# Performance work log

Measured on AMD Instinct MI355X. Metric: run time of the kernel, lower is better.

## Reference

```python
import jax, jax.numpy as jnp
import numpy as np

RADII = (0.8, 1.6)
NSAMPLES = (16, 32)
NUM_GRIDPOINTS = 216


def rotate_z(points, theta):
    # points (b, n, m, 3), theta (b, n); rotate xy about z-axis
    c = jnp.cos(theta)[:, :, None]
    s = jnp.sin(theta)[:, :, None]
    x, y, z = points[..., 0], points[..., 1], points[..., 2]
    return jnp.stack([c * x - s * y, s * x + c * y, z], axis=-1)


def ball_query(d2, radius, nsample):
    # d2: (b, Ng, K) squared distances. Returns first nsample in-radius point
    # indices per query (CUDA ball_query semantics: pad with first found index,
    # 0 if none found).
    K = d2.shape[-1]
    ar = jnp.arange(K, dtype=jnp.int32)
    scores = jnp.where(d2 < radius * radius, ar, K)  # K == sentinel for 'not in ball'
    idx = -jax.lax.top_k(-scores, nsample)[0]        # nsample smallest => first hits, ascending
    first = idx[..., :1]
    idx = jnp.where(idx >= K, first, idx)
    idx = jnp.where(idx >= K, 0, idx)
    return idx


def gather_group(xyz, feats_t, new_xyz, idx):
    # xyz (b,K,3), feats_t (b,K,C), new_xyz (b,Ng,3), idx (b,Ng,ns)
    gx = jax.vmap(lambda p, i: p[i])(xyz, idx)      # (b,Ng,ns,3)
    gf = jax.vmap(lambda f, i: f[i])(feats_t, idx)  # (b,Ng,ns,C)
    rel = gx - new_xyz[:, :, None, :]               # use_xyz=True relative coords
    return jnp.concatenate([rel, gf], axis=-1)      # (b,Ng,ns,3+C)


def setup_inputs() -> dict:
    key = jax.random.key(0)
    ks = jax.random.split(key, 12)
    b, n, m, K, C = 2, 48, NUM_GRIDPOINTS, 2048, 128
    proposals = jax.random.uniform(ks[0], (b, n, 7), dtype=jnp.float32)
    keypoint_xyz = jax.random.normal(ks[1], (b, K, 3), dtype=jnp.float32)
    keypoint_features = jax.random.normal(ks[2], (b, C, K), dtype=jnp.float32)
    grid_noise = jax.random.uniform(ks[3], (b, n, m, 3), dtype=jnp.float32)

    def lin(k, o, i):
        return jax.random.normal(k, (o, i), dtype=jnp.float32) / np.float32(np.sqrt(i))

    w0_0 = lin(ks[4], 64, C + 3)
    w0_1 = lin(ks[5], 64, 64)
    w1_0 = lin(ks[6], 64, C + 3)
    w1_1 = lin(ks[7], 64, 64)
    red_w0 = lin(ks[8], 256, 128 * m)
    red_w1 = lin(ks[9], 256, 256)
    z64 = jnp.zeros((64,), jnp.float32)
    return {
        'proposals': proposals, 'keypoint_xyz': keypoint_xyz,
        'keypoint_features': keypoint_features, 'grid_noise': grid_noise,
        'w0_0': w0_0, 'b0_0': z64, 'w0_1': w0_1, 'b0_1': z64,
        'w1_0': w1_0, 'b1_0': z64, 'w1_1': w1_1, 'b1_1': z64,
        'red_w0': red_w0, 'red_b0': jnp.zeros((256,), jnp.float32),
        'red_w1': red_w1, 'red_b1': jnp.zeros((256,), jnp.float32),
    }


def reference(proposals, keypoint_xyz, keypoint_features, grid_noise,
              w0_0, b0_0, w0_1, b0_1, w1_0, b1_0, w1_1, b1_1,
              red_w0, red_b0, red_w1, red_b1):
    b, n, _ = proposals.shape
    m = NUM_GRIDPOINTS
    # sample_gridpoints: uniform in box dims, rotate by yaw, shift to center
    grid = grid_noise * proposals[:, :, None, 3:6]
    grid = rotate_z(grid, proposals[..., 6]) + proposals[:, :, None, 0:3]
    new_xyz = grid.reshape(b, n * m, 3)                      # (b, Ng, 3)
    # squared pairwise distances via |a|^2 + |b|^2 - 2ab (avoids (b,Ng,K,3) temp)
    d2 = (jnp.sum(new_xyz * new_xyz, -1)[:, :, None]
          + jnp.sum(keypoint_xyz * keypoint_xyz, -1)[:, None, :]
          - 2.0 * jnp.einsum('bnd,bkd->bnk', new_xyz, keypoint_xyz))
    feats_t = jnp.transpose(keypoint_features, (0, 2, 1))    # (b, K, C)
    scale_params = [((w0_0, b0_0), (w0_1, b0_1)), ((w1_0, b1_0), (w1_1, b1_1))]
    outs = []
    for radius, ns, layers in zip(RADII, NSAMPLES, scale_params):
        idx = ball_query(d2, radius, ns)                     # (b, Ng, ns)
        x = gather_group(keypoint_xyz, feats_t, new_xyz, idx)  # (b, Ng, ns, 3+C)
        for W, bias in layers:                               # shared 1x1-conv MLP (BN folded)
            x = jax.nn.relu(jnp.einsum('bnsc,oc->bnso', x, W) + bias)
        outs.append(jnp.max(x, axis=2))                      # max-pool over neighbors
    x = jnp.concatenate(outs, axis=-1)                       # (b, Ng, Cout)
    Cout = x.shape[-1]
    # (b, Cout, n, m).permute(0,2,1,3).view(b, n, Cout*m) equivalent
    x = x.reshape(b, n, m, Cout).transpose(0, 1, 3, 2).reshape(b, n, Cout * m)
    x = jax.nn.relu(x @ red_w0.T + red_b0)
    x = jax.nn.relu(x @ red_w1.T + red_b1)
    return x
```

## Files before the change

kernel.cpp:

```cpp
#include <hip/hip_runtime.h>
#include <cstdint>

#define NPROP  48
#define MGRID  216
#define NPT    (NPROP*MGRID)
#define KPT    2048
#define CFEAT  128
#define R0SQ   0.64f
#define R1SQ   2.56f
#define NS0    16
#define NS1    32
#define KRED   (CFEAT*MGRID)
#define NPOINTS (2*NPT)

typedef float f32x4  __attribute__((ext_vector_type(4)));
typedef short bf16x8 __attribute__((ext_vector_type(8)));

#define AFRAG_OFF 0
#define HID_SZ    (96*256)
#define HID_OFF   8192
#define Q0_OFF    (HID_OFF + HID_SZ)
#define POOL_OFF  (Q0_OFF + 4*KPT*64)
#define W0T_OFF   (POOL_OFF + NPOINTS*CFEAT)

__device__ __forceinline__ unsigned short bf_rne(float x) {
    unsigned u = __float_as_uint(x);
    return (unsigned short)((u + 0x7fffu + ((u >> 16) & 1u)) >> 16);
}
__device__ __forceinline__ float bf_f32(unsigned short h) {
    return __uint_as_float(((unsigned)h) << 16);
}

__global__ __launch_bounds__(64) void k_wfrag(
    const float* __restrict__ w01, const float* __restrict__ w11,
    float* __restrict__ ws)
{
    int bid = blockIdx.x;
    int kc = bid & 1, ot = (bid >> 1) & 3, s = bid >> 3;
    const float* W = s ? w11 : w01;
    int l   = threadIdx.x;
    int row = ot*16 + (l & 15);
    int k0  = kc*32 + (l >> 4)*8;
    union { unsigned short u16[8]; bf16x8 v; } hh, hl;
#pragma unroll
    for (int j = 0; j < 8; ++j) {
        float x  = W[row*64 + k0 + j];
        unsigned short hi = bf_rne(x);
        float xl = x - bf_f32(hi);
        hh.u16[j] = hi;
        hl.u16[j] = bf_rne(xl);
    }
    bf16x8* Ahi = (bf16x8*)(ws + AFRAG_OFF);
    bf16x8* Alo = Ahi + 16*64;
    int fi = (s*4 + ot)*2 + kc;
    Ahi[fi*64 + l] = hh.v;
    Alo[fi*64 + l] = hl.v;
}

template <int W>
__device__ __forceinline__ void wtr_tile(const float* __restrict__ src,
                                         float* __restrict__ dst,
                                         float* __restrict__ t, int g0)
{
    const int stride = W + 1;
    for (int idx = threadIdx.x; idx < 128*W; idx += 256) {
        int c = idx / W, gg = idx - c*W;
        t[c*stride + gg] = src[c*216 + g0 + gg];
    }
    __syncthreads();
    for (int idx = threadIdx.x; idx < 128*W; idx += 256) {
        int gg = idx >> 7, c = idx & 127;
        dst[(size_t)(g0+gg)*128 + c] = t[c*stride + gg];
    }
    __syncthreads();
}

__global__ __launch_bounds__(256) void k_wtr(
    const float* __restrict__ rw0, float* __restrict__ ws)
{
    __shared__ float t[128*65];
    int o = blockIdx.x;
    const float* src = rw0 + (size_t)o*KRED;
    float* dst = ws + W0T_OFF + (size_t)o*KRED;
    wtr_tile<64>(src, dst, t, 0);
    wtr_tile<64>(src, dst, t, 64);
    wtr_tile<64>(src, dst, t, 128);
    wtr_tile<24>(src, dst, t, 192);
}

__global__ __launch_bounds__(256) void k_qproj(
    const float* __restrict__ kxyz, const float* __restrict__ feats,
    const float* __restrict__ w0, const float* __restrict__ b0,
    const float* __restrict__ w1, const float* __restrict__ b1,
    float* __restrict__ ws)
{
    __shared__ float wl[64*131];
    int bid  = blockIdx.x;
    int kgrp = bid & 511;
    int s    = (bid >> 9) & 1;
    int b    = bid >> 10;
    const float* W    = s ? w1 : w0;
    const float* bias = s ? b1 : b0;
    for (int i = threadIdx.x; i < 64*131; i += 256) wl[i] = W[i];
    __syncthreads();
    int k = kgrp*4 + (threadIdx.x >> 6);
    int o = threadIdx.x & 63;
    float acc = bias[o];
    const float* kp = kxyz + ((size_t)b*KPT + k)*3;
    acc = fmaf(wl[o*131+0], kp[0], acc);
    acc = fmaf(wl[o*131+1], kp[1], acc);
    acc = fmaf(wl[o*131+2], kp[2], acc);
    const float* f = feats + (size_t)b*CFEAT*KPT + k;
#pragma unroll 8
    for (int c = 0; c < CFEAT; ++c)
        acc = fmaf(wl[o*131+3+c], f[(size_t)c*KPT], acc);
    ws[Q0_OFF + (size_t)s*(2*KPT*64) + ((size_t)b*KPT + k)*64 + o] = acc;
}

template <int NST>
__device__ __forceinline__ void mfma_tail(
    const float* __restrict__ Qb, const bf16x8* __restrict__ Ahi,
    const bf16x8* __restrict__ Alo, const float* __restrict__ bs,
    const int* __restrict__ idxl, const float* __restrict__ u_lds,
    float* __restrict__ stage, int sbase, int lane)
{
    const int g = lane >> 4;
    bf16x8 Bhi[NST][2], Blo[NST][2];
#pragma unroll
    for (int st = 0; st < NST; ++st) {
        int sp = idxl[st*16 + (lane & 15)];
        const float* qr = Qb + ((size_t)sp << 6) + g*8;
#pragma unroll
        for (int kc = 0; kc < 2; ++kc) {
            f32x4 q0 = *(const f32x4*)(qr + kc*32);
            f32x4 q1 = *(const f32x4*)(qr + kc*32 + 4);
            f32x4 u0 = *(const f32x4*)(u_lds + kc*32 + g*8);
            f32x4 u1 = *(const f32x4*)(u_lds + kc*32 + g*8 + 4);
            union { unsigned short u16[8]; bf16x8 v; } hh, hl;
#pragma unroll
            for (int j = 0; j < 4; ++j) {
                float x = fmaxf(q0[j] - u0[j], 0.f);
                unsigned short hi = bf_rne(x);
                hh.u16[j] = hi;
                hl.u16[j] = bf_rne(x - bf_f32(hi));
                float y = fmaxf(q1[j] - u1[j], 0.f);
                unsigned short hi2 = bf_rne(y);
                hh.u16[j+4] = hi2;
                hl.u16[j+4] = bf_rne(y - bf_f32(hi2));
            }
            Bhi[st][kc] = hh.v;
            Blo[st][kc] = hl.v;
        }
    }
#pragma unroll
    for (int ot = 0; ot < 4; ++ot) {
        int fi = (sbase + ot)*2;
        bf16x8 ah0 = Ahi[(fi+0)*64 + lane];
        bf16x8 ah1 = Ahi[(fi+1)*64 + lane];
        bf16x8 al0 = Alo[(fi+0)*64 + lane];
        bf16x8 al1 = Alo[(fi+1)*64 + lane];
        f32x4 bv = *(const f32x4*)(bs + ot*16 + g*4);
        f32x4 rmax = {0.f, 0.f, 0.f, 0.f};
#pragma unroll
        for (int st = 0; st < NST; ++st) {
            f32x4 acc = {0.f, 0.f, 0.f, 0.f};
            acc = __builtin_amdgcn_mfma_f32_16x16x32_bf16(al0, Bhi[st][0], acc, 0,0,0);
            acc = __builtin_amdgcn_mfma_f32_16x16x32_bf16(al1, Bhi[st][1], acc, 0,0,0);
            acc = __builtin_amdgcn_mfma_f32_16x16x32_bf16(ah0, Blo[st][0], acc, 0,0,0);
            acc = __builtin_amdgcn_mfma_f32_16x16x32_bf16(ah1, Blo[st][1], acc, 0,0,0);
            acc = __builtin_amdgcn_mfma_f32_16x16x32_bf16(ah0, Bhi[st][0], acc, 0,0,0);
            acc = __builtin_amdgcn_mfma_f32_16x16x32_bf16(ah1, Bhi[st][1], acc, 0,0,0);
#pragma unroll
            for (int r = 0; r < 4; ++r)
                rmax[r] = fmaxf(rmax[r], fmaxf(acc[r] + bv[r], 0.f));
        }
#pragma unroll
        for (int m = 1; m < 16; m <<= 1) {
#pragma unroll
            for (int r = 0; r < 4; ++r)
                rmax[r] = fmaxf(rmax[r], __shfl_xor(rmax[r], m));
        }
        if ((lane & 15) == 0)
            *(f32x4*)(stage + ot*16 + g*4) = rmax;
    }
}

__global__ __launch_bounds__(256, 3) void k_main(
    const float* __restrict__ proposals, const float* __restrict__ kxyz,
    const float* __restrict__ grid_noise,
    const float* __restrict__ w00, const float* __restrict__ b01,
    const float* __restrict__ w10, const float* __restrict__ b11,
    float* __restrict__ ws)
{
    __shared__ int idxs[4][32];
    __shared__ __align__(16) float u_lds[4][64];
    __shared__ __align__(16) float stage[4][64];
    const int wid  = threadIdx.x >> 6;
    const int lane = threadIdx.x & 63;

    const int s = (blockIdx.x >= 5184) ? 1 : 0;
    const int p = (blockIdx.x - s*5184)*4 + wid;
    int b   = p / NPT;
    int rem = p - b*NPT;
    int i   = rem / MGRID;
    int g   = rem - i*MGRID;

    const float* Wl1 = s ? w10 : w00;
    const float* bs  = s ? b11 : b01;
    const float rsq  = s ? R1SQ : R0SQ;
    const int   ns   = s ? NS1  : NS0;

    float ax = Wl1[lane*131+0], ay = Wl1[lane*131+1], az = Wl1[lane*131+2];

    const float* pr = proposals  + ((size_t)b*NPROP + i)*7;
    const float* gn = grid_noise + (((size_t)b*NPROP + i)*MGRID + g)*3;
    float gx = gn[0]*pr[3], gy = gn[1]*pr[4], gz = gn[2]*pr[5];
    float th = pr[6];
    float ss = sinf(th), cc = cosf(th);
    float nx = cc*gx - ss*gy + pr[0];
    float ny = ss*gx + cc*gy + pr[1];
    float nz = gz + pr[2];
    float pn2 = nx*nx + ny*ny + nz*nz;
    float u = ax*nx + ay*ny + az*nz;

    int* idx = idxs[wid];
    int cnt = 0;
    const float* kb = kxyz + (size_t)b*KPT*3;
    unsigned long long ltm = (1ull << lane) - 1ull;
    for (int ck = 0; ck < KPT/64; ++ck) {
        int kk = ck*64 + lane;
        float kx = kb[kk*3+0], ky = kb[kk*3+1], kz = kb[kk*3+2];
        float kn2 = kx*kx + ky*ky + kz*kz;
        float dt  = nx*kx + ny*ky + nz*kz;
        float d2  = fmaf(-2.f, dt, pn2 + kn2);
        unsigned long long m = __ballot(d2 < rsq);
        if (m) {
            int pre = __popcll(m & ltm);
            if (((m >> lane) & 1ull) && cnt + pre < ns) idx[cnt + pre] = kk;
            cnt += __popcll(m);
            if (cnt >= ns) break;
        }
    }
    if (lane == 0 && cnt == 0) idx[0] = 0;
    u_lds[wid][lane] = u;
    asm volatile("s_waitcnt lgkmcnt(0)" ::: "memory");
    __builtin_amdgcn_wave_barrier();
    int navail = cnt ? min(cnt, ns) : 1;
    int first  = idx[0];
    if (lane >= navail && lane < ns) idx[lane] = first;
    asm volatile("s_waitcnt lgkmcnt(0)" ::: "memory");
    __builtin_amdgcn_wave_barrier();

    const float*  Qb  = ws + Q0_OFF + (size_t)s*(2*KPT*64) + (size_t)b*(KPT*64);
    const bf16x8* Ahi = (const bf16x8*)(ws + AFRAG_OFF);
    const bf16x8* Alo = Ahi + 16*64;
    if (s == 0)
        mfma_tail<1>(Qb, Ahi, Alo, bs, idx, u_lds[wid], stage[wid], 0, lane);
    else
        mfma_tail<2>(Qb, Ahi, Alo, bs, idx, u_lds[wid], stage[wid], 4, lane);

    asm volatile("s_waitcnt lgkmcnt(0)" ::: "memory");
    __builtin_amdgcn_wave_barrier();
    float mx = stage[wid][lane];

    ws[POOL_OFF + (size_t)p*CFEAT + s*64 + lane] = mx;
}

__global__ __launch_bounds__(256) void k_red0(
    const float* __restrict__ A, const float* __restrict__ w0,
    float* __restrict__ hid)
{
    __shared__ __align__(16) float Al[96*68];
    __shared__ __align__(16) float Bl[128*68];
    int bid = blockIdx.x;
    int ot  = bid & 1;
    int ks  = bid >> 1;
    int tid = threadIdx.x;
    int tx  = tid & 15, ty = tid >> 4;
    float acc[6][8] = {};

    for (int chunk = 0; chunk < 2; ++chunk) {
        int kk0 = ks*128 + chunk*64;
#pragma unroll
        for (int j = 0; j < 6; ++j) {
            int f4i = tid + j*256;
            int rr = f4i >> 4, c4 = f4i & 15;
            float4 v = *(const float4*)(A + (size_t)rr*KRED + kk0 + c4*4);
            *(float4*)(Al + rr*68 + c4*4) = v;
        }
#pragma unroll
        for (int j = 0; j < 8; ++j) {
            int f4i = tid + j*256;
            int rr = f4i >> 4, c4 = f4i & 15;
            float4 v = *(const float4*)(w0 + (size_t)(ot*128+rr)*KRED + kk0 + c4*4);
            *(float4*)(Bl + rr*68 + c4*4) = v;
        }
        __syncthreads();
#pragma unroll
        for (int k4 = 0; k4 < 16; ++k4) {
            float4 av[6], bv[8];
#pragma unroll
            for (int q = 0; q < 6; ++q) av[q] = *(const float4*)(Al + (ty*6+q)*68 + k4*4);
#pragma unroll
            for (int u = 0; u < 8; ++u) bv[u] = *(const float4*)(Bl + (u*16+tx)*68 + k4*4);
#pragma unroll
            for (int q = 0; q < 6; ++q)
#pragma unroll
                for (int u = 0; u < 8; ++u) {
                    acc[q][u] = fmaf(av[q].x, bv[u].x, acc[q][u]);
                    acc[q][u] = fmaf(av[q].y, bv[u].y, acc[q][u]);
                    acc[q][u] = fmaf(av[q].z, bv[u].z, acc[q][u]);
                    acc[q][u] = fmaf(av[q].w, bv[u].w, acc[q][u]);
                }
        }
        __syncthreads();
    }
#pragma unroll
    for (int q = 0; q < 6; ++q)
#pragma unroll
        for (int u = 0; u < 8; ++u)
            atomicAdd(hid + (size_t)(ty*6+q)*256 + ot*128 + u*16 + tx, acc[q][u]);
}

__global__ __launch_bounds__(256) void k_fin(
    const float* __restrict__ hid, const float* __restrict__ rb0,
    const float* __restrict__ w1, const float* __restrict__ rb1,
    float* __restrict__ out)
{
    __shared__ __align__(16) float hbuf[256];
    int r = blockIdx.x, o = threadIdx.x;
    float h = fmaxf(hid[(size_t)r*256 + o] + rb0[o], 0.f);
    hbuf[o] = h;
    __syncthreads();
    float a0 = rb1[o], a1 = 0.f, a2 = 0.f, a3 = 0.f;
    const float4* wrow = (const float4*)(w1 + (size_t)o*256);
    const float4* hv   = (const float4*)hbuf;
#pragma unroll 8
    for (int j = 0; j < 64; ++j) {
        float4 w = wrow[j], x = hv[j];
        a0 = fmaf(w.x, x.x, a0);
        a1 = fmaf(w.y, x.y, a1);
        a2 = fmaf(w.z, x.z, a2);
        a3 = fmaf(w.w, x.w, a3);
    }
    out[(size_t)r*256 + o] = fmaxf((a0 + a1) + (a2 + a3), 0.f);
}

extern "C" void kernel_launch(void* const* d_in, const int* in_sizes, int n_in,
                              void* d_out, int out_size, void* d_ws, size_t ws_size,
                              hipStream_t stream)
{
    (void)in_sizes; (void)n_in; (void)out_size; (void)ws_size;
    const float* proposals = (const float*)d_in[0];
    const float* kxyz      = (const float*)d_in[1];
    const float* feats     = (const float*)d_in[2];
    const float* gnoise    = (const float*)d_in[3];
    const float* w0_0 = (const float*)d_in[4];
    const float* b0_0 = (const float*)d_in[5];
    const float* w0_1 = (const float*)d_in[6];
    const float* b0_1 = (const float*)d_in[7];
    const float* w1_0 = (const float*)d_in[8];
    const float* b1_0 = (const float*)d_in[9];
    const float* w1_1 = (const float*)d_in[10];
    const float* b1_1 = (const float*)d_in[11];
    const float* rw0  = (const float*)d_in[12];
    const float* rb0  = (const float*)d_in[13];
    const float* rw1  = (const float*)d_in[14];
    const float* rb1  = (const float*)d_in[15];
    float* ws  = (float*)d_ws;
    float* out = (float*)d_out;

    hipMemsetAsync(ws + HID_OFF, 0, HID_SZ*sizeof(float), stream);
    k_wfrag<<<  16,  64, 0, stream>>>(w0_1, w1_1, ws);
    k_wtr  <<< 256, 256, 0, stream>>>(rw0, ws);
    k_qproj<<<2048, 256, 0, stream>>>(kxyz, feats, w0_0, b0_0, w1_0, b1_0, ws);
    k_main <<<10368, 256, 0, stream>>>(proposals, kxyz, gnoise,
                                       w0_0, b0_1, w1_0, b1_1, ws);
    k_red0 <<< 432, 256, 0, stream>>>(ws + POOL_OFF, ws + W0T_OFF, ws + HID_OFF);
    k_fin  <<<  96, 256, 0, stream>>>(ws + HID_OFF, rb0, rw1, rb1, out);
}
```

Baseline: 281.9 us.

## Fuse both radius scales per point, transpose pooled activations instead of weights, drop atomics

The main kernel now does the ball query for both radii in one pass over precomputed (x,y,z,|k|^2) keypoints, two chunks at a time. It then runs both MLP scales per point, which halves the block count and removes the duplicated distance scan. Instead of transposing the large reduction weight each call, the pooled features are transposed to match the original weight layout. The k-split reduction now writes partial sums to a buffer that the final kernel sums, replacing the memset and atomicAdd. In exchange there is a larger partial buffer to read, more registers in the fused main kernel, and the launch_bounds occupancy hint is dropped.

```diff
diff --git a/kernel.cpp b/kernel.cpp
--- a/kernel.cpp
+++ b/kernel.cpp
@@ -12,16 +12,18 @@
 #define NS1    32
 #define KRED   (CFEAT*MGRID)
 #define NPOINTS (2*NPT)
+#define NKSPLIT 108
 
 typedef float f32x4  __attribute__((ext_vector_type(4)));
 typedef short bf16x8 __attribute__((ext_vector_type(8)));
+typedef unsigned long long ull;
 
 #define AFRAG_OFF 0
-#define HID_SZ    (96*256)
-#define HID_OFF   8192
-#define Q0_OFF    (HID_OFF + HID_SZ)
-#define POOL_OFF  (Q0_OFF + 4*KPT*64)
-#define W0T_OFF   (POOL_OFF + NPOINTS*CFEAT)
+#define KX4_OFF   8192
+#define Q0_OFF    24576
+#define POOL_OFF  548864
+#define PT_OFF    3203072
+#define PART_OFF  5857280
 
 __device__ __forceinline__ unsigned short bf_rne(float x) {
     unsigned u = __float_as_uint(x);
@@ -31,61 +33,39 @@
     return __uint_as_float(((unsigned)h) << 16);
 }
 
-__global__ __launch_bounds__(64) void k_wfrag(
+__global__ __launch_bounds__(64) void k_pre(
+    const float* __restrict__ kxyz,
     const float* __restrict__ w01, const float* __restrict__ w11,
     float* __restrict__ ws)
 {
     int bid = blockIdx.x;
-    int kc = bid & 1, ot = (bid >> 1) & 3, s = bid >> 3;
-    const float* W = s ? w11 : w01;
-    int l   = threadIdx.x;
-    int row = ot*16 + (l & 15);
-    int k0  = kc*32 + (l >> 4)*8;
-    union { unsigned short u16[8]; bf16x8 v; } hh, hl;
-#pragma unroll
-    for (int j = 0; j < 8; ++j) {
-        float x  = W[row*64 + k0 + j];
-        unsigned short hi = bf_rne(x);
-        float xl = x - bf_f32(hi);
-        hh.u16[j] = hi;
-        hl.u16[j] = bf_rne(xl);
-    }
-    bf16x8* Ahi = (bf16x8*)(ws + AFRAG_OFF);
-    bf16x8* Alo = Ahi + 16*64;
-    int fi = (s*4 + ot)*2 + kc;
-    Ahi[fi*64 + l] = hh.v;
-    Alo[fi*64 + l] = hl.v;
-}
-
-template <int W>
-__device__ __forceinline__ void wtr_tile(const float* __restrict__ src,
-                                         float* __restrict__ dst,
-                                         float* __restrict__ t, int g0)
-{
-    const int stride = W + 1;
-    for (int idx = threadIdx.x; idx < 128*W; idx += 256) {
-        int c = idx / W, gg = idx - c*W;
-        t[c*stride + gg] = src[c*216 + g0 + gg];
-    }
-    __syncthreads();
-    for (int idx = threadIdx.x; idx < 128*W; idx += 256) {
-        int gg = idx >> 7, c = idx & 127;
-        dst[(size_t)(g0+gg)*128 + c] = t[c*stride + gg];
-    }
-    __syncthreads();
-}
-
-__global__ __launch_bounds__(256) void k_wtr(
-    const float* __restrict__ rw0, float* __restrict__ ws)
-{
-    __shared__ float t[128*65];
-    int o = blockIdx.x;
-    const float* src = rw0 + (size_t)o*KRED;
-    float* dst = ws + W0T_OFF + (size_t)o*KRED;
-    wtr_tile<64>(src, dst, t, 0);
-    wtr_tile<64>(src, dst, t, 64);
-    wtr_tile<64>(src, dst, t, 128);
-    wtr_tile<24>(src, dst, t, 192);
+    if (bid < 16) {
+        int kc = bid & 1, ot = (bid >> 1) & 3, s = bid >> 3;
+        const float* W = s ? w11 : w01;
+        int l   = threadIdx.x;
+        int row = ot*16 + (l & 15);
+        int k0  = kc*32 + (l >> 4)*8;
+        union { unsigned short u16[8]; bf16x8 v; } hh, hl;
+#pragma unroll
+        for (int j = 0; j < 8; ++j) {
+            float x  = W[row*64 + k0 + j];
+            unsigned short hi = bf_rne(x);
+            hh.u16[j] = hi;
+            hl.u16[j] = bf_rne(x - bf_f32(hi));
+        }
+        bf16x8* Ahi = (bf16x8*)(ws + AFRAG_OFF);
+        bf16x8* Alo = Ahi + 16*64;
+        int fi = (s*4 + ot)*2 + kc;
+        Ahi[fi*64 + l] = hh.v;
+        Alo[fi*64 + l] = hl.v;
+    } else {
+        int idx = (bid - 16)*64 + threadIdx.x;
+        const float* kp = kxyz + (size_t)idx*3;
+        float kx = kp[0], ky = kp[1], kz = kp[2];
+        float kn2 = fmaf(kz, kz, fmaf(ky, ky, kx*kx));
+        f32x4 v = {kx, ky, kz, kn2};
+        ((f32x4*)(ws + KX4_OFF))[idx] = v;
+    }
 }
 
 __global__ __launch_bounds__(256) void k_qproj(
@@ -118,14 +98,12 @@
 }
 
 template <int NST>
-__device__ __forceinline__ void mfma_tail(
-    const float* __restrict__ Qb, const bf16x8* __restrict__ Ahi,
-    const bf16x8* __restrict__ Alo, const float* __restrict__ bs,
-    const int* __restrict__ idxl, const float* __restrict__ u_lds,
-    float* __restrict__ stage, int sbase, int lane)
+__device__ __forceinline__ void build_bfrag(
+    const float* __restrict__ Qb, const int* __restrict__ idxl,
+    const float* __restrict__ u_lds,
+    bf16x8 (&Bhi)[NST][2], bf16x8 (&Blo)[NST][2], int lane)
 {
     const int g = lane >> 4;
-    bf16x8 Bhi[NST][2], Blo[NST][2];
 #pragma unroll
     for (int st = 0; st < NST; ++st) {
         int sp = idxl[st*16 + (lane & 15)];
@@ -152,6 +130,16 @@
             Blo[st][kc] = hl.v;
         }
     }
+}
+
+template <int NST>
+__device__ __forceinline__ void mfma_eval(
+    const bf16x8* __restrict__ Ahi, const bf16x8* __restrict__ Alo,
+    const float* __restrict__ bs,
+    const bf16x8 (&Bhi)[NST][2], const bf16x8 (&Blo)[NST][2],
+    float* __restrict__ stage, int sbase, int lane)
+{
+    const int g = lane >> 4;
 #pragma unroll
     for (int ot = 0; ot < 4; ++ot) {
         int fi = (sbase + ot)*2;
@@ -185,32 +173,27 @@
     }
 }
 
-__global__ __launch_bounds__(256, 3) void k_main(
-    const float* __restrict__ proposals, const float* __restrict__ kxyz,
-    const float* __restrict__ grid_noise,
+__global__ __launch_bounds__(256) void k_main(
+    const float* __restrict__ proposals, const float* __restrict__ grid_noise,
     const float* __restrict__ w00, const float* __restrict__ b01,
     const float* __restrict__ w10, const float* __restrict__ b11,
     float* __restrict__ ws)
 {
-    __shared__ int idxs[4][32];
-    __shared__ __align__(16) float u_lds[4][64];
+    __shared__ int idx0s[4][NS0];
+    __shared__ int idx1s[4][NS1];
+    __shared__ __align__(16) float u0l[4][64], u1l[4][64];
     __shared__ __align__(16) float stage[4][64];
     const int wid  = threadIdx.x >> 6;
     const int lane = threadIdx.x & 63;
 
-    const int s = (blockIdx.x >= 5184) ? 1 : 0;
-    const int p = (blockIdx.x - s*5184)*4 + wid;
+    const int p = blockIdx.x*4 + wid;
     int b   = p / NPT;
     int rem = p - b*NPT;
     int i   = rem / MGRID;
     int g   = rem - i*MGRID;
 
-    const float* Wl1 = s ? w10 : w00;
-    const float* bs  = s ? b11 : b01;
-    const float rsq  = s ? R1SQ : R0SQ;
-    const int   ns   = s ? NS1  : NS0;
-
-    float ax = Wl1[lane*131+0], ay = Wl1[lane*131+1], az = Wl1[lane*131+2];
+    float a0x = w00[lane*131+0], a0y = w00[lane*131+1], a0z = w00[lane*131+2];
+    float a1x = w10[lane*131+0], a1y = w10[lane*131+1], a1z = w10[lane*131+2];
 
     const float* pr = proposals  + ((size_t)b*NPROP + i)*7;
     const float* gn = grid_noise + (((size_t)b*NPROP + i)*MGRID + g)*3;
@@ -221,54 +204,110 @@
     float ny = ss*gx + cc*gy + pr[1];
     float nz = gz + pr[2];
     float pn2 = nx*nx + ny*ny + nz*nz;
-    float u = ax*nx + ay*ny + az*nz;
-
-    int* idx = idxs[wid];
-    int cnt = 0;
-    const float* kb = kxyz + (size_t)b*KPT*3;
-    unsigned long long ltm = (1ull << lane) - 1ull;
-    for (int ck = 0; ck < KPT/64; ++ck) {
-        int kk = ck*64 + lane;
-        float kx = kb[kk*3+0], ky = kb[kk*3+1], kz = kb[kk*3+2];
-        float kn2 = kx*kx + ky*ky + kz*kz;
-        float dt  = nx*kx + ny*ky + nz*kz;
-        float d2  = fmaf(-2.f, dt, pn2 + kn2);
-        unsigned long long m = __ballot(d2 < rsq);
-        if (m) {
-            int pre = __popcll(m & ltm);
-            if (((m >> lane) & 1ull) && cnt + pre < ns) idx[cnt + pre] = kk;
-            cnt += __popcll(m);
-            if (cnt >= ns) break;
-        }
-    }
-    if (lane == 0 && cnt == 0) idx[0] = 0;
-    u_lds[wid][lane] = u;
+    u0l[wid][lane] = a0x*nx + a0y*ny + a0z*nz;
+    u1l[wid][lane] = a1x*nx + a1y*ny + a1z*nz;
+
+    int* idx0 = idx0s[wid];
+    int* idx1 = idx1s[wid];
+    int cnt0 = 0, cnt1 = 0;
+    const f32x4* kx4 = (const f32x4*)(ws + KX4_OFF) + (size_t)b*KPT;
+    ull ltm = (1ull << lane) - 1ull;
+
+#define BQ_PROC(M, KK, CNT, IDX, NSV)                                         \
+    if (M) {                                                                  \
+        int pre = __popcll((M) & ltm);                                        \
+        if ((((M) >> lane) & 1ull) && CNT + pre < NSV) IDX[CNT + pre] = (KK); \
+        CNT += __popcll(M);                                                   \
+    }
+
+    for (int ck = 0; ck < KPT/64; ck += 2) {
+        f32x4 ka = kx4[ck*64 + lane];
+        f32x4 kc2 = kx4[ck*64 + 64 + lane];
+        float dta = fmaf(nz, ka.z, fmaf(ny, ka.y, nx*ka.x));
+        float d2a = fmaf(-2.f, dta, pn2 + ka.w);
+        float dtb = fmaf(nz, kc2.z, fmaf(ny, kc2.y, nx*kc2.x));
+        float d2b = fmaf(-2.f, dtb, pn2 + kc2.w);
+        ull m0a = __ballot(d2a < R0SQ);
+        ull m1a = __ballot(d2a < R1SQ);
+        ull m0b = __ballot(d2b < R0SQ);
+        ull m1b = __ballot(d2b < R1SQ);
+        int kka = ck*64 + lane, kkb = kka + 64;
+        BQ_PROC(m0a, kka, cnt0, idx0, NS0)
+        BQ_PROC(m0b, kkb, cnt0, idx0, NS0)
+        BQ_PROC(m1a, kka, cnt1, idx1, NS1)
+        BQ_PROC(m1b, kkb, cnt1, idx1, NS1)
+        if (cnt0 >= NS0 && cnt1 >= NS1) break;
+    }
+#undef BQ_PROC
+
+    if (lane == 0) {
+        if (cnt0 == 0) idx0[0] = 0;
+        if (cnt1 == 0) idx1[0] = 0;
+    }
     asm volatile("s_waitcnt lgkmcnt(0)" ::: "memory");
     __builtin_amdgcn_wave_barrier();
-    int navail = cnt ? min(cnt, ns) : 1;
-    int first  = idx[0];
-    if (lane >= navail && lane < ns) idx[lane] = first;
+    int na0 = cnt0 ? min(cnt0, NS0) : 1;
+    int na1 = cnt1 ? min(cnt1, NS1) : 1;
+    int f0 = idx0[0], f1 = idx1[0];
+    if (lane >= na0 && lane < NS0) idx0[lane] = f0;
+    if (lane >= na1 && lane < NS1) idx1[lane] = f1;
     asm volatile("s_waitcnt lgkmcnt(0)" ::: "memory");
     __builtin_amdgcn_wave_barrier();
 
-    const float*  Qb  = ws + Q0_OFF + (size_t)s*(2*KPT*64) + (size_t)b*(KPT*64);
+    const float*  Qb0 = ws + Q0_OFF + (size_t)b*(KPT*64);
+    const float*  Qb1 = ws + Q0_OFF + (size_t)(2*KPT*64) + (size_t)b*(KPT*64);
     const bf16x8* Ahi = (const bf16x8*)(ws + AFRAG_OFF);
     const bf16x8* Alo = Ahi + 16*64;
-    if (s == 0)
-        mfma_tail<1>(Qb, Ahi, Alo, bs, idx, u_lds[wid], stage[wid], 0, lane);
-    else
-        mfma_tail<2>(Qb, Ahi, Alo, bs, idx, u_lds[wid], stage[wid], 4, lane);
-
+
+    bf16x8 B0hi[1][2], B0lo[1][2], B1hi[2][2], B1lo[2][2];
+    build_bfrag<1>(Qb0, idx0, u0l[wid], B0hi, B0lo, lane);
+    build_bfrag<2>(Qb1, idx1, u1l[wid], B1hi, B1lo, lane);
+
+    mfma_eval<1>(Ahi, Alo, b01, B0hi, B0lo, stage[wid], 0, lane);
     asm volatile("s_waitcnt lgkmcnt(0)" ::: "memory");
     __builtin_amdgcn_wave_barrier();
-    float mx = stage[wid][lane];
-
-    ws[POOL_OFF + (size_t)p*CFEAT + s*64 + lane] = mx;
+    float mx0 = stage[wid][lane];
+    __builtin_amdgcn_wave_barrier();
+
+    mfma_eval<2>(Ahi, Alo, b11, B1hi, B1lo, stage[wid], 4, lane);
+    asm volatile("s_waitcnt lgkmcnt(0)" ::: "memory");
+    __builtin_amdgcn_wave_barrier();
+    float mx1 = stage[wid][lane];
+
+    ws[POOL_OFF + (size_t)p*CFEAT + lane]      = mx0;
+    ws[POOL_OFF + (size_t)p*CFEAT + 64 + lane] = mx1;
+}
+
+template <int W>
+__device__ __forceinline__ void ptr_tile(const float* __restrict__ in,
+                                         float* __restrict__ out,
+                                         float* __restrict__ t, int g0)
+{
+    for (int idx = threadIdx.x; idx < 128*W; idx += 256) {
+        int gg = idx >> 7, c = idx & 127;
+        t[c*(W+1) + gg] = in[(size_t)(g0+gg)*128 + c];
+    }
+    __syncthreads();
+    for (int idx = threadIdx.x; idx < 128*W; idx += 256) {
+        int c = idx / W, gg = idx - c*W;
+        out[c*216 + g0 + gg] = t[c*(W+1) + gg];
+    }
+}
+
+__global__ __launch_bounds__(256) void k_ptr(float* __restrict__ ws)
+{
+    __shared__ float t[128*33];
+    int bid = blockIdx.x;
+    int row = bid / 7, tt = bid - row*7;
+    const float* in = ws + POOL_OFF + (size_t)row*MGRID*CFEAT;
+    float* out = ws + PT_OFF + (size_t)row*KRED;
+    if (tt < 6) ptr_tile<32>(in, out, t, tt*32);
+    else        ptr_tile<24>(in, out, t, 192);
 }
 
 __global__ __launch_bounds__(256) void k_red0(
     const float* __restrict__ A, const float* __restrict__ w0,
-    float* __restrict__ hid)
+    float* __restrict__ part)
 {
     __shared__ __align__(16) float Al[96*68];
     __shared__ __align__(16) float Bl[128*68];
@@ -279,8 +318,8 @@
     int tx  = tid & 15, ty = tid >> 4;
     float acc[6][8] = {};
 
-    for (int chunk = 0; chunk < 2; ++chunk) {
-        int kk0 = ks*128 + chunk*64;
+    for (int chunk = 0; chunk < 4; ++chunk) {
+        int kk0 = ks*256 + chunk*64;
 #pragma unroll
         for (int j = 0; j < 6; ++j) {
             int f4i = tid + j*256;
@@ -315,21 +354,31 @@
         }
         __syncthreads();
     }
+    float* pp = part + (size_t)ks*(96*256);
 #pragma unroll
     for (int q = 0; q < 6; ++q)
 #pragma unroll
         for (int u = 0; u < 8; ++u)
-            atomicAdd(hid + (size_t)(ty*6+q)*256 + ot*128 + u*16 + tx, acc[q][u]);
+            pp[(size_t)(ty*6+q)*256 + ot*128 + u*16 + tx] = acc[q][u];
 }
 
 __global__ __launch_bounds__(256) void k_fin(
-    const float* __restrict__ hid, const float* __restrict__ rb0,
+    const float* __restrict__ part, const float* __restrict__ rb0,
     const float* __restrict__ w1, const float* __restrict__ rb1,
     float* __restrict__ out)
 {
     __shared__ __align__(16) float hbuf[256];
     int r = blockIdx.x, o = threadIdx.x;
-    float h = fmaxf(hid[(size_t)r*256 + o] + rb0[o], 0.f);
+    const float* pp = part + (size_t)r*256 + o;
+    float s0 = 0.f, s1 = 0.f, s2 = 0.f, s3 = 0.f;
+#pragma unroll 4
+    for (int ks = 0; ks < NKSPLIT; ks += 4) {
+        s0 += pp[(size_t)(ks+0)*(96*256)];
+        s1 += pp[(size_t)(ks+1)*(96*256)];
+        s2 += pp[(size_t)(ks+2)*(96*256)];
+        s3 += pp[(size_t)(ks+3)*(96*256)];
+    }
+    float h = fmaxf(((s0 + s1) + (s2 + s3)) + rb0[o], 0.f);
     hbuf[o] = h;
     __syncthreads();
     float a0 = rb1[o], a1 = 0.f, a2 = 0.f, a3 = 0.f;
@@ -370,12 +419,11 @@
     float* ws  = (float*)d_ws;
     float* out = (float*)d_out;
 
-    hipMemsetAsync(ws + HID_OFF, 0, HID_SZ*sizeof(float), stream);
-    k_wfrag<<<  16,  64, 0, stream>>>(w0_1, w1_1, ws);
-    k_wtr  <<< 256, 256, 0, stream>>>(rw0, ws);
+    k_pre  <<<  80,  64, 0, stream>>>(kxyz, w0_1, w1_1, ws);
     k_qproj<<<2048, 256, 0, stream>>>(kxyz, feats, w0_0, b0_0, w1_0, b1_0, ws);
-    k_main <<<10368, 256, 0, stream>>>(proposals, kxyz, gnoise,
-                                       w0_0, b0_1, w1_0, b1_1, ws);
-    k_red0 <<< 432, 256, 0, stream>>>(ws + POOL_OFF, ws + W0T_OFF, ws + HID_OFF);
-    k_fin  <<<  96, 256, 0, stream>>>(ws + HID_OFF, rb0, rw1, rb1, out);
-}
+    k_main <<<5184, 256, 0, stream>>>(proposals, gnoise,
+                                      w0_0, b0_1, w1_0, b1_1, ws);
+    k_ptr  <<< 672, 256, 0, stream>>>(ws);
+    k_red0 <<< 216, 256, 0, stream>>>(ws + PT_OFF, rw0, ws + PART_OFF);
+    k_fin  <<<  96, 256, 0, stream>>>(ws + PART_OFF, rb0, rw1, rb1, out);
+}
```

New measurement: 259.0 us. 8.1% less time.
